# Optimization experiments

Measured on AMD Instinct MI355X. Metric: run time of the kernel, lower is better.

The kernel has to match this reference:

```python
import jax, jax.numpy as jnp
import numpy as np

B, S, IN_DIM = 16, 1024, 64
D, H, FF, L, OUT = 512, 8, 2048, 6, 256
HD = D // H
EPS = 1e-5


def _ln(x, g, b):
    m = jnp.mean(x, axis=-1, keepdims=True)
    v = jnp.var(x, axis=-1, keepdims=True)
    return (x - m) * jax.lax.rsqrt(v + EPS) * g + b


def setup_inputs() -> dict:
    key = jax.random.key(0)
    ks = jax.random.split(key, 24)
    def rn(k, shape, scale=0.02):
        return jax.random.normal(k, shape, dtype=jnp.float32) * scale
    return {
        "x": jax.random.normal(ks[0], (B, S, IN_DIM), dtype=jnp.float32),
        "in_w": rn(ks[1], (IN_DIM, D)), "in_b": jnp.zeros((D,), jnp.float32),
        "in_ln_g": jnp.ones((D,), jnp.float32), "in_ln_b": jnp.zeros((D,), jnp.float32),
        "pos": rn(ks[2], (S, D)),
        "qkv_w": rn(ks[3], (L, D, 3 * D)), "qkv_b": jnp.zeros((L, 3 * D), jnp.float32),
        "ao_w": rn(ks[4], (L, D, D)), "ao_b": jnp.zeros((L, D), jnp.float32),
        "ff_w1": rn(ks[5], (L, D, FF)), "ff_b1": jnp.zeros((L, FF), jnp.float32),
        "ff_w2": rn(ks[6], (L, FF, D)), "ff_b2": jnp.zeros((L, D), jnp.float32),
        "ln1_g": jnp.ones((L, D), jnp.float32), "ln1_b": jnp.zeros((L, D), jnp.float32),
        "ln2_g": jnp.ones((L, D), jnp.float32), "ln2_b": jnp.zeros((L, D), jnp.float32),
        "o_w1": rn(ks[7], (D, D // 2)), "o_b1": jnp.zeros((D // 2,), jnp.float32),
        "o_ln_g": jnp.ones((D // 2,), jnp.float32), "o_ln_b": jnp.zeros((D // 2,), jnp.float32),
        "o_w2": rn(ks[8], (D // 2, OUT)), "o_b2": jnp.zeros((OUT,), jnp.float32),
    }


def reference(x, in_w, in_b, in_ln_g, in_ln_b, pos,
              qkv_w, qkv_b, ao_w, ao_b, ff_w1, ff_b1, ff_w2, ff_b2,
              ln1_g, ln1_b, ln2_g, ln2_b,
              o_w1, o_b1, o_ln_g, o_ln_b, o_w2, o_b2):
    h = x @ in_w + in_b                      # [B,S,D]
    h = _ln(h, in_ln_g, in_ln_b)
    h = h + pos[None, :, :]
    scale = 1.0 / jnp.sqrt(jnp.float32(HD))
    for l in range(L):
        qkv = h @ qkv_w[l] + qkv_b[l]        # [B,S,3D]
        q, k, v = jnp.split(qkv, 3, axis=-1)
        q = q.reshape(B, S, H, HD)
        k = k.reshape(B, S, H, HD)
        v = v.reshape(B, S, H, HD)
        scores = jnp.einsum('bqhd,bkhd->bhqk', q, k) * scale
        attn = jax.nn.softmax(scores, axis=-1)
        ctx = jnp.einsum('bhqk,bkhd->bqhd', attn, v).reshape(B, S, D)
        attn_out = ctx @ ao_w[l] + ao_b[l]
        h = _ln(h + attn_out, ln1_g[l], ln1_b[l])
        ff = jax.nn.gelu(h @ ff_w1[l] + ff_b1[l], approximate=False) @ ff_w2[l] + ff_b2[l]
        h = _ln(h + ff, ln2_g[l], ln2_b[l])
    pooled = jnp.mean(h, axis=1)             # [B,D]
    z = jax.nn.gelu(pooled @ o_w1 + o_b1, approximate=False)
    z = _ln(z, o_ln_g, o_ln_b)
    return z @ o_w2 + o_b2                   # [B,OUT]
```

## Files before the change

### kernel.cpp

```cpp
#include <hip/hip_runtime.h>
#include <hip/hip_bf16.h>

#define B_ 16
#define S_ 1024
#define IN_ 64
#define D_ 512
#define H_ 8
#define HD_ 64
#define FF_ 2048
#define L_ 6
#define OUT_ 256
#define BS_ (B_*S_)

typedef __attribute__((ext_vector_type(8))) short s16x8;
typedef __attribute__((ext_vector_type(4))) short s16x4;
typedef __attribute__((ext_vector_type(4))) float f32x4;

#define AS1(p) ((const __attribute__((address_space(1))) void*)(p))
#define AS3(p) ((__attribute__((address_space(3))) void*)(p))

__device__ __forceinline__ ushort f2bf(float x) {
  __hip_bfloat16 h = __float2bfloat16(x);
  return *reinterpret_cast<ushort*>(&h);
}
__device__ __forceinline__ float bf2f(ushort u) {
  unsigned v = ((unsigned)u) << 16;
  union { unsigned u; float f; } c; c.u = v; return c.f;
}
__device__ __forceinline__ float gelu_exact(float x) {
  return 0.5f * x * (1.0f + erff(x * 0.70710678118654752f));
}

template<int BN, int WM, int WN, int MODE>
__global__ __launch_bounds__(256)
void gemm_bt(const ushort* __restrict__ A, int lda,
             const ushort* __restrict__ Bt, int ldb,
             const float* __restrict__ bias,
             ushort* __restrict__ C, int ldc,
             int K)
{
  constexpr int BM = 128;
  constexpr int BK = 32;
  constexpr int FM = BM / (WM * 16);
  constexpr int FN = BN / (WN * 16);
  constexpr int CP = 136;
  __shared__ union {
    ushort ab[2][2][BM * BK];
    ushort c[BM * CP];
  } u;

  const int tid = threadIdx.x;
  const int lane = tid & 63;
  const int wave = tid >> 6;
  const int wr = wave / WN;
  const int wc = wave % WN;
  const int lrow = lane & 15;
  const int lk = (lane >> 4) * 8;

  const int gx = gridDim.x;
  const int nwg = gx * gridDim.y;
  const int flat = blockIdx.y * gx + blockIdx.x;
  const int T = (flat & 7) * (nwg >> 3) + (flat >> 3);
  const int m0 = (T / gx) * BM;
  const int n0 = (T % gx) * BN;

  auto stage = [&](int bi, int k0) {
#pragma unroll
    for (int rr = 0; rr < 2; ++rr) {
      int c = rr * 256 + tid;
      int row = c >> 2, cg = c & 3;
      __builtin_amdgcn_global_load_lds(
          AS1(A + (size_t)(m0 + row) * lda + k0 + cg * 8),
          AS3(u.ab[bi][0] + (size_t)(rr * 256 + wave * 64) * 8), 16, 0, 0);
    }
#pragma unroll
    for (int rr = 0; rr < 2; ++rr) {
      int c = rr * 256 + tid;
      int row = c >> 2, cg = c & 3;
      __builtin_amdgcn_global_load_lds(
          AS1(Bt + (size_t)(n0 + row) * ldb + k0 + cg * 8),
          AS3(u.ab[bi][1] + (size_t)(rr * 256 + wave * 64) * 8), 16, 0, 0);
    }
  };

  f32x4 acc[FM][FN];
#pragma unroll
  for (int m = 0; m < FM; ++m)
#pragma unroll
    for (int n = 0; n < FN; ++n)
      acc[m][n] = (f32x4){0.f, 0.f, 0.f, 0.f};

  const int nt = K / BK;
  stage(0, 0);
  for (int t = 0; t < nt; ++t) {
    const int cur = t & 1;
    if (t + 1 < nt) {
      stage(cur ^ 1, (t + 1) * BK);
      asm volatile("s_waitcnt vmcnt(4)" ::: "memory");
    } else {
      asm volatile("s_waitcnt vmcnt(0)" ::: "memory");
    }
    __builtin_amdgcn_s_barrier();
    __builtin_amdgcn_sched_barrier(0);
    const ushort* Ac = u.ab[cur][0];
    const ushort* Bc = u.ab[cur][1];
    s16x8 a[FM], b[FN];
#pragma unroll
    for (int m = 0; m < FM; ++m)
      a[m] = *(const s16x8*)&Ac[(wr * FM * 16 + m * 16 + lrow) * BK + lk];
#pragma unroll
    for (int n = 0; n < FN; ++n)
      b[n] = *(const s16x8*)&Bc[(wc * FN * 16 + n * 16 + lrow) * BK + lk];
#pragma unroll
    for (int m = 0; m < FM; ++m)
#pragma unroll
      for (int n = 0; n < FN; ++n)
        acc[m][n] = __builtin_amdgcn_mfma_f32_16x16x32_bf16(a[m], b[n], acc[m][n], 0, 0, 0);
    __builtin_amdgcn_sched_barrier(0);
    __builtin_amdgcn_s_barrier();
  }

  __syncthreads();
  const int rbL = wr * FM * 16 + (lane >> 4) * 4;
  const int cbL = wc * FN * 16 + lrow;
#pragma unroll
  for (int n = 0; n < FN; ++n) {
    int colL = cbL + n * 16;
    float bv = bias ? bias[n0 + colL] : 0.0f;
#pragma unroll
    for (int m = 0; m < FM; ++m) {
#pragma unroll
      for (int r = 0; r < 4; ++r) {
        float v = acc[m][n][r] + bv;
        if (MODE == 2) v = gelu_exact(v);
        u.c[(rbL + m * 16 + r) * CP + colL] = f2bf(v);
      }
    }
  }
  __syncthreads();
  if (MODE == 3) {
    int dl = tid >> 1, kh = tid & 1;
    int vcol = n0 + dl;
    int bb = m0 >> 10, k0r = m0 & 1023;
    ushort* vrow = C + ((size_t)(bb * 8 + (vcol >> 6)) * HD_ + (vcol & 63)) * S_
                   + k0r + kh * 64;
#pragma unroll
    for (int w2 = 0; w2 < 2; ++w2)
#pragma unroll
      for (int g2 = 0; g2 < 4; ++g2) {
        ushort outv[8];
#pragma unroll
        for (int jj = 0; jj < 8; ++jj) {
          int pk = kh * 64 + w2 * 32 + (jj < 4 ? 4 * g2 + jj : 16 + 4 * g2 + (jj - 4));
          outv[jj] = u.c[pk * CP + dl];
        }
        *(s16x8*)(vrow + w2 * 32 + g2 * 8) = *(s16x8*)outv;
      }
  } else {
#pragma unroll
    for (int p = 0; p < 8; ++p) {
      int row = p * 16 + (tid >> 4);
      int col = (tid & 15) * 8;
      s16x8 v = *(const s16x8*)&u.c[row * CP + col];
      *(s16x8*)&C[(size_t)(m0 + row) * ldc + n0 + col] = v;
    }
  }
}

__global__ __launch_bounds__(512)
void flash_kernel(const ushort* __restrict__ qkv, const ushort* __restrict__ vt,
                  ushort* __restrict__ ctx)
{
  constexpr int KB = 128;
  const float KE = 0.125f * 1.44269504f;
  __shared__ ushort ks[KB * 64];
  __shared__ ushort vs[HD_ * KB];
  const int tid = threadIdx.x;
  const int lane = tid & 63;
  const int wave = tid >> 6;
  const int lrow = lane & 15;
  const int g = lane >> 4;
  const int lk = g * 8;
  const int r7 = lrow & 7;

  const int flat = blockIdx.y * 8 + blockIdx.x;
  const int T = (flat & 7) * 128 + (flat >> 3);
  const int bh = T >> 3;
  const int b = bh >> 3, h = bh & 7;
  const int q0 = (T & 7) * 128;

  s16x8 qf[2];
  {
    const ushort* qrow = qkv + ((size_t)(b * S_ + q0 + wave * 16 + lrow)) * (3 * D_) + h * HD_;
    s16x8 r0 = *(const s16x8*)(qrow + lk);
    s16x8 r1 = *(const s16x8*)(qrow + 32 + lk);
#pragma unroll
    for (int j = 0; j < 8; ++j) {
      qf[0][j] = (short)f2bf(bf2f((ushort)r0[j]) * KE);
      qf[1][j] = (short)f2bf(bf2f((ushort)r1[j]) * KE);
    }
  }
  float lsum = 0.f;
  f32x4 o[4] = {};

  for (int kt = 0; kt < S_ / KB; ++kt) {
    __syncthreads();
#pragma unroll
    for (int r = 0; r < 2; ++r) {
      int c = r * 512 + tid;
      int row = c >> 3, cc = c & 7;
      int scc = cc ^ (row & 7);
      __builtin_amdgcn_global_load_lds(
          AS1(qkv + ((size_t)(b * S_ + kt * KB + row)) * (3 * D_) + D_ + h * HD_ + scc * 8),
          AS3(ks + (size_t)(r * 512 + wave * 64) * 8), 16, 0, 0);
    }
#pragma unroll
    for (int r = 0; r < 2; ++r) {
      int c = r * 512 + tid;
      int row = c >> 4, cc = c & 15;
      int scc = cc ^ (row & 7);
      __builtin_amdgcn_global_load_lds(
          AS1(vt + ((size_t)(bh * HD_ + row)) * S_ + kt * KB + scc * 8),
          AS3(vs + (size_t)(r * 512 + wave * 64) * 8), 16, 0, 0);
    }
    __syncthreads();

#pragma unroll
    for (int tp = 0; tp < 4; ++tp) {
      f32x4 s0 = {}, s1 = {};
      {
        int rb0 = tp * 32 + lrow;
        int rb1 = rb0 + 16;
        s16x8 k00 = *(const s16x8*)&ks[rb0 * 64 + ((g     ^ r7) * 8)];
        s16x8 k01 = *(const s16x8*)&ks[rb0 * 64 + (((g+4) ^ r7) * 8)];
        s16x8 k10 = *(const s16x8*)&ks[rb1 * 64 + ((g     ^ r7) * 8)];
        s16x8 k11 = *(const s16x8*)&ks[rb1 * 64 + (((g+4) ^ r7) * 8)];
        s0 = __builtin_amdgcn_mfma_f32_16x16x32_bf16(k00, qf[0], s0, 0, 0, 0);
        s0 = __builtin_amdgcn_mfma_f32_16x16x32_bf16(k01, qf[1], s0, 0, 0, 0);
        s1 = __builtin_amdgcn_mfma_f32_16x16x32_bf16(k10, qf[0], s1, 0, 0, 0);
        s1 = __builtin_amdgcn_mfma_f32_16x16x32_bf16(k11, qf[1], s1, 0, 0, 0);
      }
      union { s16x8 v; unsigned u[4]; } pa;
      {
        float p0 = exp2f(s0[0]), p1 = exp2f(s0[1]);
        float p2 = exp2f(s0[2]), p3 = exp2f(s0[3]);
        float p4 = exp2f(s1[0]), p5 = exp2f(s1[1]);
        float p6 = exp2f(s1[2]), p7 = exp2f(s1[3]);
        lsum += ((p0 + p1) + (p2 + p3)) + ((p4 + p5) + (p6 + p7));
        unsigned u0 = __float_as_uint(p0) + 0x8000u, u1 = __float_as_uint(p1) + 0x8000u;
        unsigned u2 = __float_as_uint(p2) + 0x8000u, u3 = __float_as_uint(p3) + 0x8000u;
        unsigned u4 = __float_as_uint(p4) + 0x8000u, u5 = __float_as_uint(p5) + 0x8000u;
        unsigned u6 = __float_as_uint(p6) + 0x8000u, u7 = __float_as_uint(p7) + 0x8000u;
        pa.u[0] = (u0 >> 16) | (u1 & 0xffff0000u);
        pa.u[1] = (u2 >> 16) | (u3 & 0xffff0000u);
        pa.u[2] = (u4 >> 16) | (u5 & 0xffff0000u);
        pa.u[3] = (u6 >> 16) | (u7 & 0xffff0000u);
      }
#pragma unroll
      for (int n2 = 0; n2 < 4; ++n2) {
        int vrow = n2 * 16 + lrow;
        s16x8 vf = *(const s16x8*)&vs[vrow * KB + (((tp * 4 + g) ^ r7) * 8)];
        o[n2] = __builtin_amdgcn_mfma_f32_16x16x32_bf16(vf, pa.v, o[n2], 0, 0, 0);
      }
    }
  }
  lsum += __shfl_xor(lsum, 16);
  lsum += __shfl_xor(lsum, 32);
  float inv = 1.0f / lsum;

  ushort* crow = ctx + ((size_t)(b * S_ + q0 + wave * 16 + lrow)) * D_ + h * HD_;
#pragma unroll
  for (int n2 = 0; n2 < 4; ++n2) {
    s16x4 w;
#pragma unroll
    for (int r = 0; r < 4; ++r) w[r] = (short)f2bf(o[n2][r] * inv);
    *(s16x4*)(crow + n2 * 16 + g * 4) = w;
  }
}

__global__ __launch_bounds__(256)
void ln512_kernel(const ushort* __restrict__ a, const ushort* __restrict__ res,
                  const float* __restrict__ g, const float* __restrict__ bt,
                  const float* __restrict__ pos,
                  ushort* __restrict__ hout)
{
  const int row = blockIdx.x;
  const int t = threadIdx.x;
  const size_t base = (size_t)row * D_;
  float x0 = bf2f(a[base + t]), x1 = bf2f(a[base + t + 256]);
  if (res) { x0 += bf2f(res[base + t]); x1 += bf2f(res[base + t + 256]); }
  float s = x0 + x1, q = x0 * x0 + x1 * x1;
#pragma unroll
  for (int m = 32; m > 0; m >>= 1) { s += __shfl_xor(s, m); q += __shfl_xor(q, m); }
  __shared__ float red[8];
  if ((t & 63) == 0) { red[(t >> 6) * 2] = s; red[(t >> 6) * 2 + 1] = q; }
  __syncthreads();
  s = red[0] + red[2] + red[4] + red[6];
  q = red[1] + red[3] + red[5] + red[7];
  float mean = s * (1.0f / D_);
  float var = q * (1.0f / D_) - mean * mean;
  float rs = rsqrtf(var + 1e-5f);
  float y0 = (x0 - mean) * rs * g[t] + bt[t];
  float y1 = (x1 - mean) * rs * g[t + 256] + bt[t + 256];
  if (pos) {
    int sp = row & (S_ - 1);
    y0 += pos[(size_t)sp * D_ + t];
    y1 += pos[(size_t)sp * D_ + t + 256];
  }
  hout[base + t] = f2bf(y0);
  hout[base + t + 256] = f2bf(y1);
}

__global__ void wtrans_kernel(const float* __restrict__ W, ushort* __restrict__ Wt, int K, int N)
{
  __shared__ float tile[32][33];
  const float* Wl = W + (size_t)blockIdx.z * K * N;
  ushort* Wtl = Wt + (size_t)blockIdx.z * K * N;
  int n0 = blockIdx.x * 32, k0 = blockIdx.y * 32;
  int tx = threadIdx.x, ty = threadIdx.y;
#pragma unroll
  for (int r = 0; r < 4; ++r)
    tile[ty * 4 + r][tx] = Wl[(size_t)(k0 + ty * 4 + r) * N + n0 + tx];
  __syncthreads();
#pragma unroll
  for (int r = 0; r < 4; ++r)
    Wtl[(size_t)(n0 + ty * 4 + r) * K + k0 + tx] = f2bf(tile[tx][ty * 4 + r]);
}

__global__ void castx_kernel(const float* __restrict__ x, ushort* __restrict__ xb, int n)
{
  int i = blockIdx.x * blockDim.x + threadIdx.x;
  if (i < n) xb[i] = f2bf(x[i]);
}

__global__ __launch_bounds__(256)
void pool_partial_kernel(const ushort* __restrict__ h, float* __restrict__ pp)
{
  int b = blockIdx.x, ch = blockIdx.y;
  int t = threadIdx.x;
  float s0 = 0, s1 = 0;
  for (int r = 0; r < 128; ++r) {
    size_t base = ((size_t)b * S_ + ch * 128 + r) * D_;
    s0 += bf2f(h[base + t]);
    s1 += bf2f(h[base + t + 256]);
  }
  pp[(size_t)(b * 8 + ch) * D_ + t] = s0;
  pp[(size_t)(b * 8 + ch) * D_ + t + 256] = s1;
}

__global__ __launch_bounds__(256)
void head_kernel(const float* __restrict__ pp,
                 const float* __restrict__ w1, const float* __restrict__ b1,
                 const float* __restrict__ lg, const float* __restrict__ lb,
                 const float* __restrict__ w2, const float* __restrict__ b2,
                 float* __restrict__ out)
{
  __shared__ float pooled[D_];
  __shared__ float z[256];
  int b = blockIdx.x, t = threadIdx.x;
  for (int i = t; i < D_; i += 256) {
    float s = 0;
    for (int c = 0; c < 8; ++c) s += pp[(size_t)(b * 8 + c) * D_ + i];
    pooled[i] = s * (1.0f / S_);
  }
  __syncthreads();
  float acc = 0;
  for (int k = 0; k < D_; ++k) acc += pooled[k] * w1[(size_t)k * 256 + t];
  float zz = gelu_exact(acc + b1[t]);
  float s = zz, q = zz * zz;
#pragma unroll
  for (int m = 32; m > 0; m >>= 1) { s += __shfl_xor(s, m); q += __shfl_xor(q, m); }
  __shared__ float red[8];
  if ((t & 63) == 0) { red[(t >> 6) * 2] = s; red[(t >> 6) * 2 + 1] = q; }
  __syncthreads();
  s = red[0] + red[2] + red[4] + red[6];
  q = red[1] + red[3] + red[5] + red[7];
  float mean = s * (1.0f / 256), var = q * (1.0f / 256) - mean * mean;
  float rs = rsqrtf(var + 1e-5f);
  z[t] = (zz - mean) * rs * lg[t] + lb[t];
  __syncthreads();
  float o = 0;
  for (int k = 0; k < 256; ++k) o += z[k] * w2[(size_t)k * 256 + t];
  out[(size_t)b * 256 + t] = o + b2[t];
}

extern "C" void kernel_launch(void* const* d_in, const int* in_sizes, int n_in,
                              void* d_out, int out_size, void* d_ws, size_t ws_size,
                              hipStream_t stream)
{
  const float* x       = (const float*)d_in[0];
  const float* in_w    = (const float*)d_in[1];
  const float* in_b    = (const float*)d_in[2];
  const float* in_ln_g = (const float*)d_in[3];
  const float* in_ln_b = (const float*)d_in[4];
  const float* pos     = (const float*)d_in[5];
  const float* qkv_w   = (const float*)d_in[6];
  const float* qkv_b   = (const float*)d_in[7];
  const float* ao_w    = (const float*)d_in[8];
  const float* ao_b    = (const float*)d_in[9];
  const float* ff_w1   = (const float*)d_in[10];
  const float* ff_b1   = (const float*)d_in[11];
  const float* ff_w2   = (const float*)d_in[12];
  const float* ff_b2   = (const float*)d_in[13];
  const float* ln1_g   = (const float*)d_in[14];
  const float* ln1_b   = (const float*)d_in[15];
  const float* ln2_g   = (const float*)d_in[16];
  const float* ln2_b   = (const float*)d_in[17];
  const float* o_w1    = (const float*)d_in[18];
  const float* o_b1    = (const float*)d_in[19];
  const float* o_ln_g  = (const float*)d_in[20];
  const float* o_ln_b  = (const float*)d_in[21];
  const float* o_w2    = (const float*)d_in[22];
  const float* o_b2    = (const float*)d_in[23];

  char* wp = (char*)d_ws;
  auto alloc = [&](size_t bytes) {
    char* p = wp;
    wp += (bytes + 255) & ~(size_t)255;
    return p;
  };
  ushort* hb     = (ushort*)alloc((size_t)BS_ * D_ * 2);
  ushort* tmpb   = (ushort*)alloc((size_t)BS_ * D_ * 2);
  ushort* big    = (ushort*)alloc((size_t)BS_ * FF_ * 2);
  ushort* ctxb   = (ushort*)alloc((size_t)BS_ * D_ * 2);
  ushort* xb     = (ushort*)alloc((size_t)BS_ * IN_ * 2);
  ushort* vt     = (ushort*)alloc((size_t)B_ * H_ * HD_ * S_ * 2);
  float*  pp     = (float*) alloc((size_t)B_ * 8 * D_ * 4);
  ushort* in_wt  = (ushort*)alloc((size_t)D_ * IN_ * 2);
  ushort* qkv_wt = (ushort*)alloc((size_t)L_ * 3 * D_ * D_ * 2);
  ushort* ao_wt  = (ushort*)alloc((size_t)L_ * D_ * D_ * 2);
  ushort* ff1_wt = (ushort*)alloc((size_t)L_ * FF_ * D_ * 2);
  ushort* ff2_wt = (ushort*)alloc((size_t)L_ * D_ * FF_ * 2);
  (void)ws_size; (void)n_in; (void)in_sizes; (void)out_size;

  dim3 wb(32, 8);
  wtrans_kernel<<<dim3(D_ / 32, IN_ / 32, 1), wb, 0, stream>>>(in_w, in_wt, IN_, D_);
  wtrans_kernel<<<dim3(3 * D_ / 32, D_ / 32, L_), wb, 0, stream>>>(qkv_w, qkv_wt, D_, 3 * D_);
  wtrans_kernel<<<dim3(D_ / 32, D_ / 32, L_), wb, 0, stream>>>(ao_w, ao_wt, D_, D_);
  wtrans_kernel<<<dim3(FF_ / 32, D_ / 32, L_), wb, 0, stream>>>(ff_w1, ff1_wt, D_, FF_);
  wtrans_kernel<<<dim3(D_ / 32, FF_ / 32, L_), wb, 0, stream>>>(ff_w2, ff2_wt, FF_, D_);
  castx_kernel<<<BS_ * IN_ / 256, 256, 0, stream>>>(x, xb, BS_ * IN_);

  gemm_bt<128, 2, 2, 1><<<dim3(D_ / 128, BS_ / 128), 256, 0, stream>>>(
      xb, IN_, in_wt, IN_, in_b, tmpb, D_, IN_);
  ln512_kernel<<<BS_, 256, 0, stream>>>(tmpb, nullptr, in_ln_g, in_ln_b, pos, hb);

  for (int l = 0; l < L_; ++l) {
    const ushort* qwt = qkv_wt + (size_t)l * 3 * D_ * D_;
    const float*  qb  = qkv_b + (size_t)l * 3 * D_;
    gemm_bt<128, 2, 2, 1><<<dim3(2 * D_ / 128, BS_ / 128), 256, 0, stream>>>(
        hb, D_, qwt, D_, qb, big, 3 * D_, D_);
    gemm_bt<128, 2, 2, 3><<<dim3(D_ / 128, BS_ / 128), 256, 0, stream>>>(
        hb, D_, qwt + (size_t)(2 * D_) * D_, D_, qb + 2 * D_, vt, S_, D_);
    flash_kernel<<<dim3(S_ / 128, B_ * H_), 512, 0, stream>>>(big, vt, ctxb);
    gemm_bt<128, 2, 2, 1><<<dim3(D_ / 128, BS_ / 128), 256, 0, stream>>>(
        ctxb, D_, ao_wt + (size_t)l * D_ * D_, D_, ao_b + (size_t)l * D_,
        tmpb, D_, D_);
    ln512_kernel<<<BS_, 256, 0, stream>>>(tmpb, hb, ln1_g + (size_t)l * D_,
                                          ln1_b + (size_t)l * D_, nullptr, hb);
    gemm_bt<128, 2, 2, 2><<<dim3(FF_ / 128, BS_ / 128), 256, 0, stream>>>(
        hb, D_, ff1_wt + (size_t)l * FF_ * D_, D_, ff_b1 + (size_t)l * FF_,
        big, FF_, D_);
    gemm_bt<128, 2, 2, 1><<<dim3(D_ / 128, BS_ / 128), 256, 0, stream>>>(
        big, FF_, ff2_wt + (size_t)l * D_ * FF_, FF_, ff_b2 + (size_t)l * D_,
        tmpb, D_, FF_);
    ln512_kernel<<<BS_, 256, 0, stream>>>(tmpb, hb, ln2_g + (size_t)l * D_,
                                          ln2_b + (size_t)l * D_, nullptr, hb);
  }
  pool_partial_kernel<<<dim3(B_, 8), 256, 0, stream>>>(hb, pp);
  head_kernel<<<B_, 256, 0, stream>>>(pp, o_w1, o_b1, o_ln_g, o_ln_b, o_w2, o_b2,
                                      (float*)d_out);
}
```

Baseline: 1.620 ms.

## Double-buffer K/V tiles in flash attention to overlap loads with MFMA

The flash attention kernel now keeps two LDS buffers for K and V tiles and issues the direct-to-LDS loads for the next key block before computing on the current one. It waits with an explicit vmcnt count so only the current tile's loads must finish, then uses raw s_barrier and sched_barrier instead of __syncthreads. The aim is to hide global load latency behind the QK and PV MFMA work. In exchange, LDS use doubles to 64KB per block, which may lower occupancy, and correctness now rests on the hand-set vmcnt values.

```diff
diff --git a/kernel.cpp b/kernel.cpp
--- a/kernel.cpp
+++ b/kernel.cpp
@@ -172,9 +172,10 @@
                   ushort* __restrict__ ctx)
 {
   constexpr int KB = 128;
+  constexpr int NT = S_ / KB;
   const float KE = 0.125f * 1.44269504f;
-  __shared__ ushort ks[KB * 64];
-  __shared__ ushort vs[HD_ * KB];
+  __shared__ ushort ks[2][KB * 64];
+  __shared__ ushort vs[2][HD_ * KB];
   const int tid = threadIdx.x;
   const int lane = tid & 63;
   const int wave = tid >> 6;
@@ -200,11 +201,8 @@
       qf[1][j] = (short)f2bf(bf2f((ushort)r1[j]) * KE);
     }
   }
-  float lsum = 0.f;
-  f32x4 o[4] = {};
-
-  for (int kt = 0; kt < S_ / KB; ++kt) {
-    __syncthreads();
+
+  auto stage = [&](int bi, int kt) {
 #pragma unroll
     for (int r = 0; r < 2; ++r) {
       int c = r * 512 + tid;
@@ -212,7 +210,7 @@
       int scc = cc ^ (row & 7);
       __builtin_amdgcn_global_load_lds(
           AS1(qkv + ((size_t)(b * S_ + kt * KB + row)) * (3 * D_) + D_ + h * HD_ + scc * 8),
-          AS3(ks + (size_t)(r * 512 + wave * 64) * 8), 16, 0, 0);
+          AS3(ks[bi] + (size_t)(r * 512 + wave * 64) * 8), 16, 0, 0);
     }
 #pragma unroll
     for (int r = 0; r < 2; ++r) {
@@ -221,9 +219,26 @@
       int scc = cc ^ (row & 7);
       __builtin_amdgcn_global_load_lds(
           AS1(vt + ((size_t)(bh * HD_ + row)) * S_ + kt * KB + scc * 8),
-          AS3(vs + (size_t)(r * 512 + wave * 64) * 8), 16, 0, 0);
-    }
-    __syncthreads();
+          AS3(vs[bi] + (size_t)(r * 512 + wave * 64) * 8), 16, 0, 0);
+    }
+  };
+
+  float lsum = 0.f;
+  f32x4 o[4] = {};
+
+  stage(0, 0);
+  for (int kt = 0; kt < NT; ++kt) {
+    const int cur = kt & 1;
+    if (kt + 1 < NT) {
+      stage(cur ^ 1, kt + 1);
+      asm volatile("s_waitcnt vmcnt(4)" ::: "memory");
+    } else {
+      asm volatile("s_waitcnt vmcnt(0)" ::: "memory");
+    }
+    __builtin_amdgcn_s_barrier();
+    __builtin_amdgcn_sched_barrier(0);
+    const ushort* kp = ks[cur];
+    const ushort* vp = vs[cur];
 
 #pragma unroll
     for (int tp = 0; tp < 4; ++tp) {
@@ -231,10 +246,10 @@
       {
         int rb0 = tp * 32 + lrow;
         int rb1 = rb0 + 16;
-        s16x8 k00 = *(const s16x8*)&ks[rb0 * 64 + ((g     ^ r7) * 8)];
-        s16x8 k01 = *(const s16x8*)&ks[rb0 * 64 + (((g+4) ^ r7) * 8)];
-        s16x8 k10 = *(const s16x8*)&ks[rb1 * 64 + ((g     ^ r7) * 8)];
-        s16x8 k11 = *(const s16x8*)&ks[rb1 * 64 + (((g+4) ^ r7) * 8)];
+        s16x8 k00 = *(const s16x8*)&kp[rb0 * 64 + ((g     ^ r7) * 8)];
+        s16x8 k01 = *(const s16x8*)&kp[rb0 * 64 + (((g+4) ^ r7) * 8)];
+        s16x8 k10 = *(const s16x8*)&kp[rb1 * 64 + ((g     ^ r7) * 8)];
+        s16x8 k11 = *(const s16x8*)&kp[rb1 * 64 + (((g+4) ^ r7) * 8)];
         s0 = __builtin_amdgcn_mfma_f32_16x16x32_bf16(k00, qf[0], s0, 0, 0, 0);
         s0 = __builtin_amdgcn_mfma_f32_16x16x32_bf16(k01, qf[1], s0, 0, 0, 0);
         s1 = __builtin_amdgcn_mfma_f32_16x16x32_bf16(k10, qf[0], s1, 0, 0, 0);
@@ -259,10 +274,12 @@
 #pragma unroll
       for (int n2 = 0; n2 < 4; ++n2) {
         int vrow = n2 * 16 + lrow;
-        s16x8 vf = *(const s16x8*)&vs[vrow * KB + (((tp * 4 + g) ^ r7) * 8)];
+        s16x8 vf = *(const s16x8*)&vp[vrow * KB + (((tp * 4 + g) ^ r7) * 8)];
         o[n2] = __builtin_amdgcn_mfma_f32_16x16x32_bf16(vf, pa.v, o[n2], 0, 0, 0);
       }
     }
+    __builtin_amdgcn_sched_barrier(0);
+    __builtin_amdgcn_s_barrier();
   }
   lsum += __shfl_xor(lsum, 16);
   lsum += __shfl_xor(lsum, 32);
```

Result: no change. 1.632 ms (+0.7%).

## Process two query tiles per flash block to reuse K/V tiles

Applied to the files above, without the earlier changes.

Each flash attention block now handles 256 queries (two 128-query sub-tiles per wave) instead of 128, and the grid is halved. The K and V fragments loaded into shared memory and registers are reused for both query sub-tiles, which halves global K/V traffic and LDS reads per query. The cost is more registers per thread (two sets of Q fragments, accumulators and partial sums), which may lower occupancy. Fewer blocks (512) also means fewer waves to hide latency across the GPU's compute units.

```diff
diff --git a/kernel.cpp b/kernel.cpp
--- a/kernel.cpp
+++ b/kernel.cpp
@@ -183,25 +183,27 @@
   const int lk = g * 8;
   const int r7 = lrow & 7;
 
-  const int flat = blockIdx.y * 8 + blockIdx.x;
-  const int T = (flat & 7) * 128 + (flat >> 3);
-  const int bh = T >> 3;
+  const int flat = blockIdx.y * 4 + blockIdx.x;
+  const int T = (flat & 7) * 64 + (flat >> 3);
+  const int bh = T >> 2;
   const int b = bh >> 3, h = bh & 7;
-  const int q0 = (T & 7) * 128;
-
-  s16x8 qf[2];
-  {
-    const ushort* qrow = qkv + ((size_t)(b * S_ + q0 + wave * 16 + lrow)) * (3 * D_) + h * HD_;
+  const int q0 = (T & 3) * 256;
+
+  s16x8 qf[2][2];
+#pragma unroll
+  for (int qq = 0; qq < 2; ++qq) {
+    const ushort* qrow = qkv +
+        ((size_t)(b * S_ + q0 + qq * 128 + wave * 16 + lrow)) * (3 * D_) + h * HD_;
     s16x8 r0 = *(const s16x8*)(qrow + lk);
     s16x8 r1 = *(const s16x8*)(qrow + 32 + lk);
 #pragma unroll
     for (int j = 0; j < 8; ++j) {
-      qf[0][j] = (short)f2bf(bf2f((ushort)r0[j]) * KE);
-      qf[1][j] = (short)f2bf(bf2f((ushort)r1[j]) * KE);
-    }
-  }
-  float lsum = 0.f;
-  f32x4 o[4] = {};
+      qf[qq][0][j] = (short)f2bf(bf2f((ushort)r0[j]) * KE);
+      qf[qq][1][j] = (short)f2bf(bf2f((ushort)r1[j]) * KE);
+    }
+  }
+  float lsum0 = 0.f, lsum1 = 0.f;
+  f32x4 o[2][4] = {};
 
   for (int kt = 0; kt < S_ / KB; ++kt) {
     __syncthreads();
@@ -227,54 +229,79 @@
 
 #pragma unroll
     for (int tp = 0; tp < 4; ++tp) {
-      f32x4 s0 = {}, s1 = {};
+      int rb0 = tp * 32 + lrow;
+      int rb1 = rb0 + 16;
+      s16x8 k00 = *(const s16x8*)&ks[rb0 * 64 + ((g     ^ r7) * 8)];
+      s16x8 k01 = *(const s16x8*)&ks[rb0 * 64 + (((g+4) ^ r7) * 8)];
+      s16x8 k10 = *(const s16x8*)&ks[rb1 * 64 + ((g     ^ r7) * 8)];
+      s16x8 k11 = *(const s16x8*)&ks[rb1 * 64 + (((g+4) ^ r7) * 8)];
+      union { s16x8 v; unsigned u[4]; } pa0, pa1;
       {
-        int rb0 = tp * 32 + lrow;
-        int rb1 = rb0 + 16;
-        s16x8 k00 = *(const s16x8*)&ks[rb0 * 64 + ((g     ^ r7) * 8)];
-        s16x8 k01 = *(const s16x8*)&ks[rb0 * 64 + (((g+4) ^ r7) * 8)];
-        s16x8 k10 = *(const s16x8*)&ks[rb1 * 64 + ((g     ^ r7) * 8)];
-        s16x8 k11 = *(const s16x8*)&ks[rb1 * 64 + (((g+4) ^ r7) * 8)];
-        s0 = __builtin_amdgcn_mfma_f32_16x16x32_bf16(k00, qf[0], s0, 0, 0, 0);
-        s0 = __builtin_amdgcn_mfma_f32_16x16x32_bf16(k01, qf[1], s0, 0, 0, 0);
-        s1 = __builtin_amdgcn_mfma_f32_16x16x32_bf16(k10, qf[0], s1, 0, 0, 0);
-        s1 = __builtin_amdgcn_mfma_f32_16x16x32_bf16(k11, qf[1], s1, 0, 0, 0);
-      }
-      union { s16x8 v; unsigned u[4]; } pa;
-      {
+        f32x4 s0 = {}, s1 = {};
+        s0 = __builtin_amdgcn_mfma_f32_16x16x32_bf16(k00, qf[0][0], s0, 0, 0, 0);
+        s0 = __builtin_amdgcn_mfma_f32_16x16x32_bf16(k01, qf[0][1], s0, 0, 0, 0);
+        s1 = __builtin_amdgcn_mfma_f32_16x16x32_bf16(k10, qf[0][0], s1, 0, 0, 0);
+        s1 = __builtin_amdgcn_mfma_f32_16x16x32_bf16(k11, qf[0][1], s1, 0, 0, 0);
         float p0 = exp2f(s0[0]), p1 = exp2f(s0[1]);
         float p2 = exp2f(s0[2]), p3 = exp2f(s0[3]);
         float p4 = exp2f(s1[0]), p5 = exp2f(s1[1]);
         float p6 = exp2f(s1[2]), p7 = exp2f(s1[3]);
-        lsum += ((p0 + p1) + (p2 + p3)) + ((p4 + p5) + (p6 + p7));
+        lsum0 += ((p0 + p1) + (p2 + p3)) + ((p4 + p5) + (p6 + p7));
         unsigned u0 = __float_as_uint(p0) + 0x8000u, u1 = __float_as_uint(p1) + 0x8000u;
         unsigned u2 = __float_as_uint(p2) + 0x8000u, u3 = __float_as_uint(p3) + 0x8000u;
         unsigned u4 = __float_as_uint(p4) + 0x8000u, u5 = __float_as_uint(p5) + 0x8000u;
         unsigned u6 = __float_as_uint(p6) + 0x8000u, u7 = __float_as_uint(p7) + 0x8000u;
-        pa.u[0] = (u0 >> 16) | (u1 & 0xffff0000u);
-        pa.u[1] = (u2 >> 16) | (u3 & 0xffff0000u);
-        pa.u[2] = (u4 >> 16) | (u5 & 0xffff0000u);
-        pa.u[3] = (u6 >> 16) | (u7 & 0xffff0000u);
+        pa0.u[0] = (u0 >> 16) | (u1 & 0xffff0000u);
+        pa0.u[1] = (u2 >> 16) | (u3 & 0xffff0000u);
+        pa0.u[2] = (u4 >> 16) | (u5 & 0xffff0000u);
+        pa0.u[3] = (u6 >> 16) | (u7 & 0xffff0000u);
+      }
+      {
+        f32x4 s0 = {}, s1 = {};
+        s0 = __builtin_amdgcn_mfma_f32_16x16x32_bf16(k00, qf[1][0], s0, 0, 0, 0);
+        s0 = __builtin_amdgcn_mfma_f32_16x16x32_bf16(k01, qf[1][1], s0, 0, 0, 0);
+        s1 = __builtin_amdgcn_mfma_f32_16x16x32_bf16(k10, qf[1][0], s1, 0, 0, 0);
+        s1 = __builtin_amdgcn_mfma_f32_16x16x32_bf16(k11, qf[1][1], s1, 0, 0, 0);
+        float p0 = exp2f(s0[0]), p1 = exp2f(s0[1]);
+        float p2 = exp2f(s0[2]), p3 = exp2f(s0[3]);
+        float p4 = exp2f(s1[0]), p5 = exp2f(s1[1]);
+        float p6 = exp2f(s1[2]), p7 = exp2f(s1[3]);
+        lsum1 += ((p0 + p1) + (p2 + p3)) + ((p4 + p5) + (p6 + p7));
+        unsigned u0 = __float_as_uint(p0) + 0x8000u, u1 = __float_as_uint(p1) + 0x8000u;
+        unsigned u2 = __float_as_uint(p2) + 0x8000u, u3 = __float_as_uint(p3) + 0x8000u;
+        unsigned u4 = __float_as_uint(p4) + 0x8000u, u5 = __float_as_uint(p5) + 0x8000u;
+        unsigned u6 = __float_as_uint(p6) + 0x8000u, u7 = __float_as_uint(p7) + 0x8000u;
+        pa1.u[0] = (u0 >> 16) | (u1 & 0xffff0000u);
+        pa1.u[1] = (u2 >> 16) | (u3 & 0xffff0000u);
+        pa1.u[2] = (u4 >> 16) | (u5 & 0xffff0000u);
+        pa1.u[3] = (u6 >> 16) | (u7 & 0xffff0000u);
       }
 #pragma unroll
       for (int n2 = 0; n2 < 4; ++n2) {
         int vrow = n2 * 16 + lrow;
         s16x8 vf = *(const s16x8*)&vs[vrow * KB + (((tp * 4 + g) ^ r7) * 8)];
-        o[n2] = __builtin_amdgcn_mfma_f32_16x16x32_bf16(vf, pa.v, o[n2], 0, 0, 0);
+        o[0][n2] = __builtin_amdgcn_mfma_f32_16x16x32_bf16(vf, pa0.v, o[0][n2], 0, 0, 0);
+        o[1][n2] = __builtin_amdgcn_mfma_f32_16x16x32_bf16(vf, pa1.v, o[1][n2], 0, 0, 0);
       }
     }
   }
-  lsum += __shfl_xor(lsum, 16);
-  lsum += __shfl_xor(lsum, 32);
-  float inv = 1.0f / lsum;
-
-  ushort* crow = ctx + ((size_t)(b * S_ + q0 + wave * 16 + lrow)) * D_ + h * HD_;
-#pragma unroll
-  for (int n2 = 0; n2 < 4; ++n2) {
-    s16x4 w;
-#pragma unroll
-    for (int r = 0; r < 4; ++r) w[r] = (short)f2bf(o[n2][r] * inv);
-    *(s16x4*)(crow + n2 * 16 + g * 4) = w;
+  lsum0 += __shfl_xor(lsum0, 16);
+  lsum0 += __shfl_xor(lsum0, 32);
+  lsum1 += __shfl_xor(lsum1, 16);
+  lsum1 += __shfl_xor(lsum1, 32);
+
+#pragma unroll
+  for (int qq = 0; qq < 2; ++qq) {
+    float inv = 1.0f / (qq ? lsum1 : lsum0);
+    ushort* crow = ctx +
+        ((size_t)(b * S_ + q0 + qq * 128 + wave * 16 + lrow)) * D_ + h * HD_;
+#pragma unroll
+    for (int n2 = 0; n2 < 4; ++n2) {
+      s16x4 w;
+#pragma unroll
+      for (int r = 0; r < 4; ++r) w[r] = (short)f2bf(o[qq][n2][r] * inv);
+      *(s16x4*)(crow + n2 * 16 + g * 4) = w;
+    }
   }
 }
 
@@ -452,7 +479,7 @@
         hb, D_, qwt, D_, qb, big, 3 * D_, D_);
     gemm_bt<128, 2, 2, 3><<<dim3(D_ / 128, BS_ / 128), 256, 0, stream>>>(
         hb, D_, qwt + (size_t)(2 * D_) * D_, D_, qb + 2 * D_, vt, S_, D_);
-    flash_kernel<<<dim3(S_ / 128, B_ * H_), 512, 0, stream>>>(big, vt, ctxb);
+    flash_kernel<<<dim3(S_ / 256, B_ * H_), 512, 0, stream>>>(big, vt, ctxb);
     gemm_bt<128, 2, 2, 1><<<dim3(D_ / 128, BS_ / 128), 256, 0, stream>>>(
         ctxb, D_, ao_wt + (size_t)l * D_ * D_, D_, ao_b + (size_t)l * D_,
         tmpb, D_, D_);
```

Result: slower. 1.673 ms (+3.3%).
